# Performance work log

Measured on AMD Instinct MI355X. Metric: run time of the kernel, lower is better.

## Reference

```python
import jax, jax.numpy as jnp
import numpy as np

D_MODEL = 1024
NUM_HEADS = 16
D_K = D_MODEL // NUM_HEADS
LN_EPS = 1e-5
NEG = -1000000000.0


def setup_inputs() -> dict:
    key = jax.random.key(0)
    ks = jax.random.split(key, 9)
    B, S = 2, 2048
    scale = 1.0 / np.sqrt(D_MODEL)
    Q = jax.random.normal(ks[0], (B, S, D_MODEL), jnp.float32)
    K = jax.random.normal(ks[1], (B, S, D_MODEL), jnp.float32)
    V = jax.random.normal(ks[2], (B, S, D_MODEL), jnp.float32)
    # causal mask: 0 = blocked (future), 1 = attend
    mask = jnp.broadcast_to(jnp.tril(jnp.ones((S, S), jnp.int32)), (B, S, S))
    W_Q = jax.random.normal(ks[3], (D_MODEL, D_MODEL), jnp.float32) * scale
    W_K = jax.random.normal(ks[4], (D_MODEL, D_MODEL), jnp.float32) * scale
    W_V = jax.random.normal(ks[5], (D_MODEL, D_MODEL), jnp.float32) * scale
    W_O = jax.random.normal(ks[6], (D_MODEL, D_MODEL), jnp.float32) * scale
    ln_gamma = jnp.ones((D_MODEL,), jnp.float32)
    ln_beta = jnp.zeros((D_MODEL,), jnp.float32)
    return {"Q": Q, "K": K, "V": V, "mask": mask,
            "W_Q": W_Q, "W_K": W_K, "W_V": W_V, "W_O": W_O,
            "ln_gamma": ln_gamma, "ln_beta": ln_beta}


def _layer_norm(x, gamma, beta):
    mu = jnp.mean(x, axis=-1, keepdims=True)
    var = jnp.mean(jnp.square(x - mu), axis=-1, keepdims=True)
    return (x - mu) * jax.lax.rsqrt(var + LN_EPS) * gamma + beta


def reference(Q, K, V, mask, W_Q, W_K, W_V, W_O, ln_gamma, ln_beta):
    B, S, _ = Q.shape
    residual = Q
    # torch Linear: y = x @ W.T ; split into heads -> [B, H, S, d_k]
    q = (Q @ W_Q.T).reshape(B, S, NUM_HEADS, D_K).transpose(0, 2, 1, 3)
    k = (K @ W_K.T).reshape(B, S, NUM_HEADS, D_K).transpose(0, 2, 1, 3)
    v = (V @ W_V.T).reshape(B, S, NUM_HEADS, D_K).transpose(0, 2, 1, 3)
    scores = jnp.einsum('bhqd,bhkd->bhqk', q, k) / np.sqrt(D_K)
    scores = jnp.where(mask[:, None, :, :] == 0, NEG, scores)
    attn_weights = jax.nn.softmax(scores, axis=-1)  # [B, H, S, S]
    attn_out = jnp.einsum('bhqk,bhkd->bhqd', attn_weights, v)
    attn_out = attn_out.transpose(0, 2, 1, 3).reshape(B, S, D_MODEL)
    out = attn_out @ W_O.T
    out = _layer_norm(out + residual, ln_gamma, ln_beta)
    return out, attn_weights
```

## Files before the change

### kernel.cpp

```cpp
#include <hip/hip_runtime.h>
#include <cstdint>
#include <cstddef>

#define D_MODEL 1024
#define NHEADS  16
#define DKH     64
#define BB      2
#define SS      2048
#define MM      (BB*SS)

typedef short bf16x8 __attribute__((ext_vector_type(8)));
typedef float f32x4  __attribute__((ext_vector_type(4)));

#define MFMA(a,b,c) __builtin_amdgcn_mfma_f32_16x16x32_bf16(a,b,c,0,0,0)

__device__ __forceinline__ unsigned short f2bf(float f) {
    unsigned int u = __float_as_uint(f);
    u += 0x7FFFu + ((u >> 16) & 1u);
    return (unsigned short)(u >> 16);
}

__device__ __forceinline__ void gld16(const unsigned short* g, char* l) {
    __builtin_amdgcn_global_load_lds((const __attribute__((address_space(1))) void*)g,
                                     (__attribute__((address_space(3))) void*)l, 16, 0, 0);
}

template<int NISS>
__device__ __forceinline__ void stage128(char* ldsbase, const unsigned short* gorig,
                                         long gstride, int w, int l) {
#pragma unroll
    for (int is = 0; is < NISS; ++is) {
        const int pb = is * 4096 + w * 1024 + l * 16;
        const int lb = pb ^ (((pb >> 7) & 7) << 4);
        gld16(gorig + (long)(lb >> 7) * gstride + ((lb & 127) >> 1),
              ldsbase + is * 4096 + w * 1024);
    }
}

__device__ __forceinline__ bf16x8 fld(const char* lds, int row, int kb) {
    int lofs = row * 128 + kb;
    lofs ^= ((row & 7) << 4);
    return *(const bf16x8*)(lds + lofs);
}

__global__ __launch_bounds__(256)
void k_cvt(const float* __restrict__ Q, const float* __restrict__ K,
           const float* __restrict__ V, const float* __restrict__ WQ,
           const float* __restrict__ WK, const float* __restrict__ WV,
           const float* __restrict__ WO, unsigned short* __restrict__ dst)
{
    const size_t i8 = ((size_t)blockIdx.x * 256 + threadIdx.x) * 8;
    const size_t C = 4194304;
    const float* src; size_t off;
    if (i8 < C)          { src = Q; off = i8; }
    else if (i8 < 2 * C) { src = K; off = i8 - C; }
    else if (i8 < 3 * C) { src = V; off = i8 - 2 * C; }
    else {
        const size_t t = i8 - 3 * C;
        const size_t wi = t >> 20;
        off = t & 1048575;
        src = (wi == 0) ? WQ : (wi == 1) ? WK : (wi == 2) ? WV : WO;
    }
    const float4 f0 = ((const float4*)(src + off))[0];
    const float4 f1 = ((const float4*)(src + off))[1];
    bf16x8 v;
    v[0] = (short)f2bf(f0.x); v[1] = (short)f2bf(f0.y);
    v[2] = (short)f2bf(f0.z); v[3] = (short)f2bf(f0.w);
    v[4] = (short)f2bf(f1.x); v[5] = (short)f2bf(f1.y);
    v[6] = (short)f2bf(f1.z); v[7] = (short)f2bf(f1.w);
    *(bf16x8*)(dst + i8) = v;
}

template<int MODE>
__global__ __launch_bounds__(256)
void k_gemm(const unsigned short* __restrict__ A, const unsigned short* __restrict__ B,
            unsigned short* __restrict__ obf, const float* __restrict__ resid,
            float* __restrict__ ofp)
{
    __shared__ char lds[32768];
    const int tid = threadIdx.x;
    const int w = tid >> 6, l = tid & 63;
    const int n0 = blockIdx.x * 128, m0 = blockIdx.y * 128;
    const int wr = (w >> 1) * 64, wc = (w & 1) * 64;

    f32x4 acc[4][4] = {};

    for (int kt = 0; kt < 16; ++kt) {
        __syncthreads();
        stage128<4>(lds,         A + (size_t)m0 * 1024 + kt * 64, 1024, w, l);
        stage128<4>(lds + 16384, B + (size_t)n0 * 1024 + kt * 64, 1024, w, l);
        __syncthreads();
#pragma unroll
        for (int ks = 0; ks < 2; ++ks) {
            const int kb = ks * 64 + (l >> 4) * 16;
            bf16x8 av[4], bv[4];
#pragma unroll
            for (int i = 0; i < 4; ++i) av[i] = fld(lds,         wr + i * 16 + (l & 15), kb);
#pragma unroll
            for (int j = 0; j < 4; ++j) bv[j] = fld(lds + 16384, wc + j * 16 + (l & 15), kb);
#pragma unroll
            for (int i = 0; i < 4; ++i)
#pragma unroll
                for (int j = 0; j < 4; ++j)
                    acc[i][j] = MFMA(av[i], bv[j], acc[i][j]);
        }
    }

#pragma unroll
    for (int i = 0; i < 4; ++i)
#pragma unroll
        for (int j = 0; j < 4; ++j)
#pragma unroll
            for (int r = 0; r < 4; ++r) {
                const int m = m0 + wr + i * 16 + ((l >> 4) << 2) + r;
                const int n = n0 + wc + j * 16 + (l & 15);
                const float v = acc[i][j][r];
                if (MODE == 0) {
                    const int b = m >> 11, s = m & 2047, h = n >> 6, dk = n & 63;
                    obf[((size_t)(b * 16 + h) * 2048 + s) * 64 + dk] = f2bf(v);
                } else if (MODE == 1) {
                    const int b = m >> 11, s = m & 2047, h = n >> 6, dk = n & 63;
                    obf[((size_t)(b * 16 + h) * 64 + dk) * 2048 + s] = f2bf(v);
                } else {
                    const size_t o = (size_t)m * 1024 + n;
                    ofp[o] = v + resid[o];
                }
            }
}

__global__ __launch_bounds__(256)
void k_attn(const unsigned short* __restrict__ Qh, const unsigned short* __restrict__ Kh,
            float* __restrict__ attn, unsigned short* __restrict__ P)
{
    __shared__ char Qs[8192];
    __shared__ char Ks[8192];
    const int tid = threadIdx.x, w = tid >> 6, l = tid & 63;
    const int qt = blockIdx.x, bh = blockIdx.y;
    const int i0 = qt * 64;
    const unsigned short* qb = Qh + (size_t)bh * SS * DKH;
    const unsigned short* kb = Kh + (size_t)bh * SS * DKH;
    float*          ab = attn + (size_t)bh * SS * SS;
    unsigned short* pb = P    + (size_t)bh * SS * SS;

    stage128<2>(Qs, qb + (size_t)i0 * DKH, DKH, w, l);
    __syncthreads();
    bf16x8 qa[2];
#pragma unroll
    for (int ks = 0; ks < 2; ++ks)
        qa[ks] = fld(Qs, w * 16 + (l & 15), ks * 64 + (l >> 4) * 16);

    float m4[4], l4[4];
#pragma unroll
    for (int r = 0; r < 4; ++r) { m4[r] = -3.0e38f; l4[r] = 0.f; }

    const int qrow = i0 + w * 16 + ((l >> 4) << 2);

    for (int kt = 0; kt <= qt; ++kt) {
        __syncthreads();
        stage128<2>(Ks, kb + (size_t)kt * 64 * DKH, DKH, w, l);
        __syncthreads();
        f32x4 sc[4] = {};
#pragma unroll
        for (int ks = 0; ks < 2; ++ks) {
            const int kbyt = ks * 64 + (l >> 4) * 16;
#pragma unroll
            for (int n = 0; n < 4; ++n) {
                bf16x8 bv = fld(Ks, n * 16 + (l & 15), kbyt);
                sc[n] = MFMA(qa[ks], bv, sc[n]);
            }
        }
#pragma unroll
        for (int n = 0; n < 4; ++n) {
            const int kp = kt * 64 + n * 16 + (l & 15);
#pragma unroll
            for (int r = 0; r < 4; ++r) {
                float s = sc[n][r] * 0.125f;
                if (kt == qt && kp > qrow + r) s = -3.0e38f;
                sc[n][r] = s;
            }
        }
        float tm[4], ts[4];
#pragma unroll
        for (int r = 0; r < 4; ++r)
            tm[r] = fmaxf(fmaxf(sc[0][r], sc[1][r]), fmaxf(sc[2][r], sc[3][r]));
#pragma unroll
        for (int off = 1; off < 16; off <<= 1)
#pragma unroll
            for (int r = 0; r < 4; ++r) tm[r] = fmaxf(tm[r], __shfl_xor(tm[r], off));
#pragma unroll
        for (int r = 0; r < 4; ++r) {
            const float mn = fmaxf(m4[r], tm[r]);
            const float e0 = __expf(sc[0][r] - mn), e1 = __expf(sc[1][r] - mn);
            const float e2 = __expf(sc[2][r] - mn), e3 = __expf(sc[3][r] - mn);
            ts[r] = (e0 + e1) + (e2 + e3);
            l4[r] *= __expf(m4[r] - mn);
            m4[r] = mn;
        }
#pragma unroll
        for (int off = 1; off < 16; off <<= 1)
#pragma unroll
            for (int r = 0; r < 4; ++r) ts[r] += __shfl_xor(ts[r], off);
#pragma unroll
        for (int r = 0; r < 4; ++r) l4[r] += ts[r];
    }

    float inv[4];
#pragma unroll
    for (int r = 0; r < 4; ++r) inv[r] = 1.0f / l4[r];

    for (int kt = 0; kt <= qt; ++kt) {
        __syncthreads();
        stage128<2>(Ks, kb + (size_t)kt * 64 * DKH, DKH, w, l);
        __syncthreads();
        f32x4 sc[4] = {};
#pragma unroll
        for (int ks = 0; ks < 2; ++ks) {
            const int kbyt = ks * 64 + (l >> 4) * 16;
#pragma unroll
            for (int n = 0; n < 4; ++n) {
                bf16x8 bv = fld(Ks, n * 16 + (l & 15), kbyt);
                sc[n] = MFMA(qa[ks], bv, sc[n]);
            }
        }
#pragma unroll
        for (int n = 0; n < 4; ++n) {
            const int kp = kt * 64 + n * 16 + (l & 15);
#pragma unroll
            for (int r = 0; r < 4; ++r) {
                float s = sc[n][r] * 0.125f;
                if (kt == qt && kp > qrow + r) s = -3.0e38f;
                const float wgt = __expf(s - m4[r]) * inv[r];
                ab[(size_t)(qrow + r) * SS + kp] = wgt;
                pb[(size_t)(qrow + r) * SS + kp] = f2bf(wgt);
            }
        }
    }

    const int zs = (qt + 1) * 64;
    if (zs < SS) {
        const int rl = tid >> 2;
        float4* row = (float4*)(ab + (size_t)(i0 + rl) * SS);
        for (int c = (zs >> 2) + (tid & 3); c < SS / 4; c += 4)
            row[c] = make_float4(0.f, 0.f, 0.f, 0.f);
    }
}

__global__ __launch_bounds__(256)
void k_pv(const unsigned short* __restrict__ P, const unsigned short* __restrict__ VT,
          unsigned short* __restrict__ ctx)
{
    __shared__ char Ps[8192];
    __shared__ char Vs[8192];
    const int tid = threadIdx.x, w = tid >> 6, l = tid & 63;
    const int qt = blockIdx.x, bh = blockIdx.y;
    const int i0 = qt * 64;
    const unsigned short* pbase = P  + (size_t)bh * SS * SS + (size_t)i0 * SS;
    const unsigned short* vbase = VT + (size_t)bh * DKH * SS;

    f32x4 acc[4] = {};
    for (int kt = 0; kt <= qt; ++kt) {
        __syncthreads();
        stage128<2>(Ps, pbase + kt * 64, SS, w, l);
        stage128<2>(Vs, vbase + kt * 64, SS, w, l);
        __syncthreads();
#pragma unroll
        for (int ks = 0; ks < 2; ++ks) {
            const int kbyt = ks * 64 + (l >> 4) * 16;
            const bf16x8 a = fld(Ps, w * 16 + (l & 15), kbyt);
#pragma unroll
            for (int n = 0; n < 4; ++n) {
                const bf16x8 b = fld(Vs, n * 16 + (l & 15), kbyt);
                acc[n] = MFMA(a, b, acc[n]);
            }
        }
    }
    const int b = bh >> 4, h = bh & 15;
    const int qrow = i0 + w * 16 + ((l >> 4) << 2);
#pragma unroll
    for (int n = 0; n < 4; ++n)
#pragma unroll
        for (int r = 0; r < 4; ++r) {
            const int dk = n * 16 + (l & 15);
            ctx[(size_t)(b * SS + qrow + r) * D_MODEL + h * DKH + dk] = f2bf(acc[n][r]);
        }
}

__global__ __launch_bounds__(256)
void k_ln(const float* __restrict__ pre, const float* __restrict__ gamma,
          const float* __restrict__ beta, float* __restrict__ out)
{
    const int row = blockIdx.x;
    const int tid = threadIdx.x;
    const float* p = pre + (size_t)row * D_MODEL;
    float* o = out + (size_t)row * D_MODEL;

    __shared__ float red[4];

    float4 x = ((const float4*)p)[tid];
    float s = x.x + x.y + x.z + x.w;
#pragma unroll
    for (int off = 32; off; off >>= 1) s += __shfl_down(s, off);
    if ((tid & 63) == 0) red[tid >> 6] = s;
    __syncthreads();
    const float mu = (red[0] + red[1] + red[2] + red[3]) * (1.0f / D_MODEL);

    float dx[4] = {x.x - mu, x.y - mu, x.z - mu, x.w - mu};
    float ss = dx[0] * dx[0] + dx[1] * dx[1] + dx[2] * dx[2] + dx[3] * dx[3];
#pragma unroll
    for (int off = 32; off; off >>= 1) ss += __shfl_down(ss, off);
    __syncthreads();
    if ((tid & 63) == 0) red[tid >> 6] = ss;
    __syncthreads();
    const float var = (red[0] + red[1] + red[2] + red[3]) * (1.0f / D_MODEL);
    const float inv = rsqrtf(var + 1e-5f);

    const float4 g  = ((const float4*)gamma)[tid];
    const float4 be = ((const float4*)beta)[tid];
    ((float4*)o)[tid] = make_float4(dx[0] * inv * g.x + be.x, dx[1] * inv * g.y + be.y,
                                    dx[2] * inv * g.z + be.z, dx[3] * inv * g.w + be.w);
}

extern "C" void kernel_launch(void* const* d_in, const int* in_sizes, int n_in,
                              void* d_out, int out_size, void* d_ws, size_t ws_size,
                              hipStream_t stream)
{
    const float* Q     = (const float*)d_in[0];
    const float* K     = (const float*)d_in[1];
    const float* V     = (const float*)d_in[2];
    const float* WQ    = (const float*)d_in[4];
    const float* WK    = (const float*)d_in[5];
    const float* WV    = (const float*)d_in[6];
    const float* WO    = (const float*)d_in[7];
    const float* gamma = (const float*)d_in[8];
    const float* beta  = (const float*)d_in[9];

    float* out  = (float*)d_out;
    float* attn = out + (size_t)BB * SS * D_MODEL;

    char* ws = (char*)d_ws;
    unsigned short* cvt = (unsigned short*)ws;
    unsigned short* Xq = cvt;
    unsigned short* Xk = cvt + 4194304;
    unsigned short* Xv = cvt + 2 * 4194304;
    unsigned short* Wq = cvt + 3 * 4194304;
    unsigned short* Wk = Wq + 1048576;
    unsigned short* Wv = Wk + 1048576;
    unsigned short* Wo = Wv + 1048576;
    unsigned short* Qh  = (unsigned short*)(ws + 33554432);
    unsigned short* Kh  = Qh + 4194304;
    unsigned short* VhT = Kh + 4194304;
    unsigned short* Pb  = (unsigned short*)(ws + 58720256);
    unsigned short* ctx = (unsigned short*)(ws + 58720256 + 268435456);
    float*          pre = (float*)(ws + 58720256 + 268435456 + 8388608);

    k_cvt<<<dim3(8192), dim3(256), 0, stream>>>(Q, K, V, WQ, WK, WV, WO, cvt);
    k_gemm<0><<<dim3(8, 32), dim3(256), 0, stream>>>(Xq, Wq, Qh, nullptr, nullptr);
    k_gemm<0><<<dim3(8, 32), dim3(256), 0, stream>>>(Xk, Wk, Kh, nullptr, nullptr);
    k_gemm<1><<<dim3(8, 32), dim3(256), 0, stream>>>(Xv, Wv, VhT, nullptr, nullptr);
    k_attn<<<dim3(32, 32), dim3(256), 0, stream>>>(Qh, Kh, attn, Pb);
    k_pv<<<dim3(32, 32), dim3(256), 0, stream>>>(Pb, VhT, ctx);
    k_gemm<2><<<dim3(8, 32), dim3(256), 0, stream>>>(ctx, Wo, nullptr, Q, pre);
    k_ln<<<dim3(MM), dim3(256), 0, stream>>>(pre, gamma, beta, out);
}
```

Before: 890.1 us.

## Fuse PV into attention kernel and batch QKV projections into one launch

Result: faster. 844.6 us (-5.1%).

```diff
diff --git a/kernel.cpp b/kernel.cpp
--- a/kernel.cpp
+++ b/kernel.cpp
@@ -10,6 +10,7 @@
 #define MM      (BB*SS)
 
 typedef short bf16x8 __attribute__((ext_vector_type(8)));
+typedef short bf16x4 __attribute__((ext_vector_type(4)));
 typedef float f32x4  __attribute__((ext_vector_type(4)));
 
 #define MFMA(a,b,c) __builtin_amdgcn_mfma_f32_16x16x32_bf16(a,b,c,0,0,0)
@@ -18,6 +19,9 @@
     unsigned int u = __float_as_uint(f);
     u += 0x7FFFu + ((u >> 16) & 1u);
     return (unsigned short)(u >> 16);
+}
+__device__ __forceinline__ float bf2f(unsigned short u) {
+    return __uint_as_float(((unsigned int)u) << 16);
 }
 
 __device__ __forceinline__ void gld16(const unsigned short* g, char* l) {
@@ -71,13 +75,19 @@
     *(bf16x8*)(dst + i8) = v;
 }
 
-template<int MODE>
 __global__ __launch_bounds__(256)
-void k_gemm(const unsigned short* __restrict__ A, const unsigned short* __restrict__ B,
-            unsigned short* __restrict__ obf, const float* __restrict__ resid,
-            float* __restrict__ ofp)
+void k_qkv(const unsigned short* __restrict__ Xq, const unsigned short* __restrict__ Xk,
+           const unsigned short* __restrict__ Xv, const unsigned short* __restrict__ Wq,
+           const unsigned short* __restrict__ Wk, const unsigned short* __restrict__ Wv,
+           unsigned short* __restrict__ Qh, unsigned short* __restrict__ Kh,
+           unsigned short* __restrict__ VhT)
 {
     __shared__ char lds[32768];
+    const int z = blockIdx.z;
+    const unsigned short* __restrict__ A = (z == 0) ? Xq : (z == 1) ? Xk : Xv;
+    const unsigned short* __restrict__ B = (z == 0) ? Wq : (z == 1) ? Wk : Wv;
+    unsigned short* __restrict__ O       = (z == 0) ? Qh : (z == 1) ? Kh : VhT;
+
     const int tid = threadIdx.x;
     const int w = tid >> 6, l = tid & 63;
     const int n0 = blockIdx.x * 128, m0 = blockIdx.y * 128;
@@ -114,33 +124,30 @@
             for (int r = 0; r < 4; ++r) {
                 const int m = m0 + wr + i * 16 + ((l >> 4) << 2) + r;
                 const int n = n0 + wc + j * 16 + (l & 15);
-                const float v = acc[i][j][r];
-                if (MODE == 0) {
-                    const int b = m >> 11, s = m & 2047, h = n >> 6, dk = n & 63;
-                    obf[((size_t)(b * 16 + h) * 2048 + s) * 64 + dk] = f2bf(v);
-                } else if (MODE == 1) {
-                    const int b = m >> 11, s = m & 2047, h = n >> 6, dk = n & 63;
-                    obf[((size_t)(b * 16 + h) * 64 + dk) * 2048 + s] = f2bf(v);
-                } else {
-                    const size_t o = (size_t)m * 1024 + n;
-                    ofp[o] = v + resid[o];
-                }
+                const int b = m >> 11, s = m & 2047, h = n >> 6, dk = n & 63;
+                const unsigned short bv = f2bf(acc[i][j][r]);
+                if (z < 2) O[((size_t)(b * 16 + h) * 2048 + s) * 64 + dk] = bv;
+                else       O[((size_t)(b * 16 + h) * 64 + dk) * 2048 + s] = bv;
             }
 }
 
 __global__ __launch_bounds__(256)
 void k_attn(const unsigned short* __restrict__ Qh, const unsigned short* __restrict__ Kh,
-            float* __restrict__ attn, unsigned short* __restrict__ P)
+            const unsigned short* __restrict__ VhT, float* __restrict__ attn,
+            unsigned short* __restrict__ ctx)
 {
     __shared__ char Qs[8192];
     __shared__ char Ks[8192];
+    __shared__ char Vs[8192];
+    __shared__ char Ps[8192];
+
     const int tid = threadIdx.x, w = tid >> 6, l = tid & 63;
     const int qt = blockIdx.x, bh = blockIdx.y;
     const int i0 = qt * 64;
-    const unsigned short* qb = Qh + (size_t)bh * SS * DKH;
-    const unsigned short* kb = Kh + (size_t)bh * SS * DKH;
-    float*          ab = attn + (size_t)bh * SS * SS;
-    unsigned short* pb = P    + (size_t)bh * SS * SS;
+    const unsigned short* qb = Qh  + (size_t)bh * SS * DKH;
+    const unsigned short* kb = Kh  + (size_t)bh * SS * DKH;
+    const unsigned short* vb = VhT + (size_t)bh * DKH * SS;
+    float* ab = attn + (size_t)bh * SS * SS;
 
     stage128<2>(Qs, qb + (size_t)i0 * DKH, DKH, w, l);
     __syncthreads();
@@ -164,10 +171,8 @@
         for (int ks = 0; ks < 2; ++ks) {
             const int kbyt = ks * 64 + (l >> 4) * 16;
 #pragma unroll
-            for (int n = 0; n < 4; ++n) {
-                bf16x8 bv = fld(Ks, n * 16 + (l & 15), kbyt);
-                sc[n] = MFMA(qa[ks], bv, sc[n]);
-            }
+            for (int n = 0; n < 4; ++n)
+                sc[n] = MFMA(qa[ks], fld(Ks, n * 16 + (l & 15), kbyt), sc[n]);
         }
 #pragma unroll
         for (int n = 0; n < 4; ++n) {
@@ -208,81 +213,136 @@
 #pragma unroll
     for (int r = 0; r < 4; ++r) inv[r] = 1.0f / l4[r];
 
+    f32x4 acc_o[4] = {};
+
     for (int kt = 0; kt <= qt; ++kt) {
         __syncthreads();
         stage128<2>(Ks, kb + (size_t)kt * 64 * DKH, DKH, w, l);
+        stage128<2>(Vs, vb + kt * 64, SS, w, l);
         __syncthreads();
         f32x4 sc[4] = {};
 #pragma unroll
         for (int ks = 0; ks < 2; ++ks) {
             const int kbyt = ks * 64 + (l >> 4) * 16;
 #pragma unroll
-            for (int n = 0; n < 4; ++n) {
-                bf16x8 bv = fld(Ks, n * 16 + (l & 15), kbyt);
-                sc[n] = MFMA(qa[ks], bv, sc[n]);
-            }
+            for (int n = 0; n < 4; ++n)
+                sc[n] = MFMA(qa[ks], fld(Ks, n * 16 + (l & 15), kbyt), sc[n]);
         }
 #pragma unroll
         for (int n = 0; n < 4; ++n) {
-            const int kp = kt * 64 + n * 16 + (l & 15);
+            const int col = n * 16 + (l & 15);
+            const int kp = kt * 64 + col;
 #pragma unroll
             for (int r = 0; r < 4; ++r) {
                 float s = sc[n][r] * 0.125f;
                 if (kt == qt && kp > qrow + r) s = -3.0e38f;
                 const float wgt = __expf(s - m4[r]) * inv[r];
-                ab[(size_t)(qrow + r) * SS + kp] = wgt;
-                pb[(size_t)(qrow + r) * SS + kp] = f2bf(wgt);
+                const int row = w * 16 + ((l >> 4) << 2) + r;
+                int ofs = row * 128 + col * 2;
+                ofs ^= ((row & 7) << 4);
+                *(unsigned short*)(Ps + ofs) = f2bf(wgt);
             }
         }
+        __syncthreads();
+#pragma unroll
+        for (int ks = 0; ks < 2; ++ks) {
+            const int kbyt = ks * 64 + (l >> 4) * 16;
+            const bf16x8 pa = fld(Ps, w * 16 + (l & 15), kbyt);
+#pragma unroll
+            for (int n = 0; n < 4; ++n)
+                acc_o[n] = MFMA(pa, fld(Vs, n * 16 + (l & 15), kbyt), acc_o[n]);
+        }
+#pragma unroll
+        for (int rp = 0; rp < 4; ++rp) {
+            const int row = rp * 16 + (tid >> 4);
+            int ofs = row * 128 + (tid & 15) * 8;
+            ofs ^= ((row & 7) << 4);
+            const bf16x4 pv4 = *(const bf16x4*)(Ps + ofs);
+            float4 f;
+            f.x = bf2f((unsigned short)pv4[0]); f.y = bf2f((unsigned short)pv4[1]);
+            f.z = bf2f((unsigned short)pv4[2]); f.w = bf2f((unsigned short)pv4[3]);
+            *(float4*)(ab + (size_t)(i0 + row) * SS + kt * 64 + (tid & 15) * 4) = f;
+        }
+    }
+
+    __syncthreads();
+#pragma unroll
+    for (int n = 0; n < 4; ++n) {
+        const int col = n * 16 + (l & 15);
+#pragma unroll
+        for (int r = 0; r < 4; ++r) {
+            const int row = w * 16 + ((l >> 4) << 2) + r;
+            int ofs = row * 128 + col * 2;
+            ofs ^= ((row & 7) << 4);
+            *(unsigned short*)(Ps + ofs) = f2bf(acc_o[n][r]);
+        }
+    }
+    __syncthreads();
+    const int b = bh >> 4, h = bh & 15;
+#pragma unroll
+    for (int rp = 0; rp < 4; ++rp) {
+        const int row = rp * 16 + (tid >> 4);
+        int ofs = row * 128 + (tid & 15) * 8;
+        ofs ^= ((row & 7) << 4);
+        const bf16x4 o4 = *(const bf16x4*)(Ps + ofs);
+        *(bf16x4*)(ctx + (size_t)(b * SS + i0 + row) * D_MODEL + h * DKH + (tid & 15) * 4) = o4;
     }
 
     const int zs = (qt + 1) * 64;
     if (zs < SS) {
-        const int rl = tid >> 2;
-        float4* row = (float4*)(ab + (size_t)(i0 + rl) * SS);
-        for (int c = (zs >> 2) + (tid & 3); c < SS / 4; c += 4)
-            row[c] = make_float4(0.f, 0.f, 0.f, 0.f);
+        const int nf4 = (SS - zs) >> 2;
+        const float4 z4 = make_float4(0.f, 0.f, 0.f, 0.f);
+        for (int r = 0; r < 64; ++r) {
+            float4* dst = (float4*)(ab + (size_t)(i0 + r) * SS + zs);
+            for (int c = tid; c < nf4; c += 256) dst[c] = z4;
+        }
     }
 }
 
 __global__ __launch_bounds__(256)
-void k_pv(const unsigned short* __restrict__ P, const unsigned short* __restrict__ VT,
-          unsigned short* __restrict__ ctx)
-{
-    __shared__ char Ps[8192];
-    __shared__ char Vs[8192];
-    const int tid = threadIdx.x, w = tid >> 6, l = tid & 63;
-    const int qt = blockIdx.x, bh = blockIdx.y;
-    const int i0 = qt * 64;
-    const unsigned short* pbase = P  + (size_t)bh * SS * SS + (size_t)i0 * SS;
-    const unsigned short* vbase = VT + (size_t)bh * DKH * SS;
-
-    f32x4 acc[4] = {};
-    for (int kt = 0; kt <= qt; ++kt) {
-        __syncthreads();
-        stage128<2>(Ps, pbase + kt * 64, SS, w, l);
-        stage128<2>(Vs, vbase + kt * 64, SS, w, l);
+void k_oproj(const unsigned short* __restrict__ A, const unsigned short* __restrict__ B,
+             const float* __restrict__ resid, float* __restrict__ ofp)
+{
+    __shared__ char lds[32768];
+    const int tid = threadIdx.x;
+    const int w = tid >> 6, l = tid & 63;
+    const int n0 = blockIdx.x * 128, m0 = blockIdx.y * 128;
+    const int wr = (w >> 1) * 64, wc = (w & 1) * 64;
+
+    f32x4 acc[4][4] = {};
+
+    for (int kt = 0; kt < 16; ++kt) {
+        __syncthreads();
+        stage128<4>(lds,         A + (size_t)m0 * 1024 + kt * 64, 1024, w, l);
+        stage128<4>(lds + 16384, B + (size_t)n0 * 1024 + kt * 64, 1024, w, l);
         __syncthreads();
 #pragma unroll
         for (int ks = 0; ks < 2; ++ks) {
-            const int kbyt = ks * 64 + (l >> 4) * 16;
-            const bf16x8 a = fld(Ps, w * 16 + (l & 15), kbyt);
-#pragma unroll
-            for (int n = 0; n < 4; ++n) {
-                const bf16x8 b = fld(Vs, n * 16 + (l & 15), kbyt);
-                acc[n] = MFMA(a, b, acc[n]);
+            const int kb = ks * 64 + (l >> 4) * 16;
+            bf16x8 av[4], bv[4];
+#pragma unroll
+            for (int i = 0; i < 4; ++i) av[i] = fld(lds,         wr + i * 16 + (l & 15), kb);
+#pragma unroll
+            for (int j = 0; j < 4; ++j) bv[j] = fld(lds + 16384, wc + j * 16 + (l & 15), kb);
+#pragma unroll
+            for (int i = 0; i < 4; ++i)
+#pragma unroll
+                for (int j = 0; j < 4; ++j)
+                    acc[i][j] = MFMA(av[i], bv[j], acc[i][j]);
+        }
+    }
+
+#pragma unroll
+    for (int i = 0; i < 4; ++i)
+#pragma unroll
+        for (int j = 0; j < 4; ++j)
+#pragma unroll
+            for (int r = 0; r < 4; ++r) {
+                const int m = m0 + wr + i * 16 + ((l >> 4) << 2) + r;
+                const int n = n0 + wc + j * 16 + (l & 15);
+                const size_t o = (size_t)m * 1024 + n;
+                ofp[o] = acc[i][j][r] + resid[o];
             }
-        }
-    }
-    const int b = bh >> 4, h = bh & 15;
-    const int qrow = i0 + w * 16 + ((l >> 4) << 2);
-#pragma unroll
-    for (int n = 0; n < 4; ++n)
-#pragma unroll
-        for (int r = 0; r < 4; ++r) {
-            const int dk = n * 16 + (l & 15);
-            ctx[(size_t)(b * SS + qrow + r) * D_MODEL + h * DKH + dk] = f2bf(acc[n][r]);
-        }
 }
 
 __global__ __launch_bounds__(256)
@@ -349,16 +409,12 @@
     unsigned short* Qh  = (unsigned short*)(ws + 33554432);
     unsigned short* Kh  = Qh + 4194304;
     unsigned short* VhT = Kh + 4194304;
-    unsigned short* Pb  = (unsigned short*)(ws + 58720256);
-    unsigned short* ctx = (unsigned short*)(ws + 58720256 + 268435456);
-    float*          pre = (float*)(ws + 58720256 + 268435456 + 8388608);
+    unsigned short* ctx = (unsigned short*)(ws + 58720256);
+    float*          pre = (float*)(ws + 67108864);
 
     k_cvt<<<dim3(8192), dim3(256), 0, stream>>>(Q, K, V, WQ, WK, WV, WO, cvt);
-    k_gemm<0><<<dim3(8, 32), dim3(256), 0, stream>>>(Xq, Wq, Qh, nullptr, nullptr);
-    k_gemm<0><<<dim3(8, 32), dim3(256), 0, stream>>>(Xk, Wk, Kh, nullptr, nullptr);
-    k_gemm<1><<<dim3(8, 32), dim3(256), 0, stream>>>(Xv, Wv, VhT, nullptr, nullptr);
-    k_attn<<<dim3(32, 32), dim3(256), 0, stream>>>(Qh, Kh, attn, Pb);
-    k_pv<<<dim3(32, 32), dim3(256), 0, stream>>>(Pb, VhT, ctx);
-    k_gemm<2><<<dim3(8, 32), dim3(256), 0, stream>>>(ctx, Wo, nullptr, Q, pre);
+    k_qkv<<<dim3(8, 32, 3), dim3(256), 0, stream>>>(Xq, Xk, Xv, Wq, Wk, Wv, Qh, Kh, VhT);
+    k_attn<<<dim3(32, 32), dim3(256), 0, stream>>>(Qh, Kh, VhT, attn, ctx);
+    k_oproj<<<dim3(8, 32), dim3(256), 0, stream>>>(ctx, Wo, Q, pre);
     k_ln<<<dim3(MM), dim3(256), 0, stream>>>(pre, gamma, beta, out);
 }
```
